# Optimization experiments

Measured on AMD Instinct MI355X. Metric: run time of the kernel, lower is better.

## Reference

```python
import jax, jax.numpy as jnp
import numpy as np

N = 50000      # nodes
E = 100000     # edges
F_NODE = 128
F_EDGE = 16
H = 64         # hidden_dim
OUT = 32
STEPS = 3
G = 64         # num_graphs (static; batch.max()+1 in torch)


def setup_inputs() -> dict:
    key = jax.random.key(0)
    ks = jax.random.split(key, 20)

    def lin(k, fin, fout):
        s = 1.0 / np.sqrt(fin)
        return jax.random.uniform(k, (fin, fout), jnp.float32, -s, s)

    def bias(k, fin, fout):
        s = 1.0 / np.sqrt(fin)
        return jax.random.uniform(k, (fout,), jnp.float32, -s, s)

    inp = {
        'x': jax.random.normal(ks[0], (N, F_NODE), jnp.float32),
        'edge_index': jax.random.randint(ks[1], (2, E), 0, N),
        'edge_attr': jax.random.normal(ks[2], (E, F_EDGE), jnp.float32),
        'batch': jnp.sort(jax.random.randint(ks[3], (N,), 0, G)),
        # node encoder
        'W_enc': lin(ks[4], F_NODE, H), 'b_enc': bias(ks[5], F_NODE, H),
        # edge_nn: Linear(F_EDGE,H) -> ReLU -> Linear(H, H*H)
        'W_e1': lin(ks[6], F_EDGE, H), 'b_e1': bias(ks[7], F_EDGE, H),
        'W_e2': lin(ks[8], H, H * H), 'b_e2': bias(ks[9], H, H * H),
        # GRUCell (torch layout: [3H, H])
        'W_ih': jax.random.uniform(ks[10], (3 * H, H), jnp.float32, -1/np.sqrt(H), 1/np.sqrt(H)),
        'W_hh': jax.random.uniform(ks[11], (3 * H, H), jnp.float32, -1/np.sqrt(H), 1/np.sqrt(H)),
        'b_ih': jax.random.uniform(ks[12], (3 * H,), jnp.float32, -1/np.sqrt(H), 1/np.sqrt(H)),
        'b_hh': jax.random.uniform(ks[13], (3 * H,), jnp.float32, -1/np.sqrt(H), 1/np.sqrt(H)),
        # readout MLP: Linear(H,H) -> ReLU -> Linear(H,OUT)
        'W_r1': lin(ks[14], H, H), 'b_r1': bias(ks[15], H, H),
        'W_r2': lin(ks[16], H, OUT), 'b_r2': bias(ks[17], H, OUT),
    }
    return inp


def gru_cell(m, h, W_ih, W_hh, b_ih, b_hh):
    gi = m @ W_ih.T + b_ih   # [N, 3H]
    gh = h @ W_hh.T + b_hh
    i_r, i_z, i_n = jnp.split(gi, 3, axis=-1)
    h_r, h_z, h_n = jnp.split(gh, 3, axis=-1)
    r = jax.nn.sigmoid(i_r + h_r)
    z = jax.nn.sigmoid(i_z + h_z)
    n = jnp.tanh(i_n + r * h_n)
    return (1.0 - z) * n + z * h


def reference(x, edge_index, edge_attr, batch, W_enc, b_enc, W_e1, b_e1,
              W_e2, b_e2, W_ih, W_hh, b_ih, b_hh, W_r1, b_r1, W_r2, b_r2):
    h = x @ W_enc + b_enc                                   # [N, H]
    src, dst = edge_index[0], edge_index[1]
    # edge-conditioned weight matrices (loop-invariant; compute once)
    ew = (jax.nn.relu(edge_attr @ W_e1 + b_e1) @ W_e2 + b_e2).reshape(E, H, H)
    for _ in range(STEPS):
        msg = jnp.einsum('eij,ej->ei', ew, h[src])          # per-edge matvec
        m_agg = jax.ops.segment_sum(msg, dst, num_segments=N)
        h = gru_cell(m_agg, h, W_ih, W_hh, b_ih, b_hh)
    g = jax.ops.segment_sum(h, batch, num_segments=G)       # sum readout
    return jax.nn.relu(g @ W_r1 + b_r1) @ W_r2 + b_r2
```

## Files before the change

### kernel.cpp

```cpp
#include <hip/hip_runtime.h>
#include <hip/hip_fp16.h>
#include <math.h>

#define NN 50000
#define NE 100000
#define FN 128
#define FE 16
#define HD 64
#define OUTD 32
#define NG 64
#define ZK 65
#define EB 256

typedef unsigned int uint;
typedef unsigned short ushort;
typedef __attribute__((ext_vector_type(8))) short short8;
typedef __attribute__((ext_vector_type(8))) _Float16 half8;
typedef __attribute__((ext_vector_type(2))) _Float16 half2v;
typedef __attribute__((ext_vector_type(16))) float f32x16;

static __device__ __forceinline__ ushort f2h(float f) {
    _Float16 h = (_Float16)f;
    return __builtin_bit_cast(ushort, h);
}
static __device__ __forceinline__ uint pkh2(float a, float b) {
    auto r = __builtin_amdgcn_cvt_pkrtz(a, b);
    return __builtin_bit_cast(uint, r);
}
static __device__ __forceinline__ uint hmul2u(uint a, uint b) {
    half2v x = __builtin_bit_cast(half2v, a);
    half2v y = __builtin_bit_cast(half2v, b);
    half2v r = x * y;
    return __builtin_bit_cast(uint, r);
}
static __device__ __forceinline__ half8 u4h8(uint4 u) {
    return __builtin_bit_cast(half8, u);
}
static __device__ __forceinline__ float fsigmoid(float x) {
    return 1.f / (1.f + __expf(-x));
}
static __device__ __forceinline__ float ftanh(float x) {
    float t = __expf(2.f * x);
    return 1.f - 2.f / (t + 1.f);
}

#define PREP_S0 (ZK * 4096)
#define PREP_S1 (256 * 128)
#define PREP_S2 (64 * 128)
__global__ void k_prep(const float* __restrict__ W_e2, const float* __restrict__ b_e2,
                       const float* __restrict__ W_ih, const float* __restrict__ W_hh,
                       const float* __restrict__ W_enc,
                       ushort* __restrict__ Wtb, ushort* __restrict__ Bg,
                       ushort* __restrict__ Wet) {
    int idx = blockIdx.x * 256 + threadIdx.x;
    if (idx < PREP_S0) {
        int k0 = idx >> 12, r = idx & 4095;
        int i = r >> 6, j = r & 63;
        float v = (k0 < 64) ? W_e2[k0 * 4096 + i * 64 + j] : b_e2[i * 64 + j];
        Wtb[idx] = f2h(v);
        return;
    }
    idx -= PREP_S0;
    if (idx < PREP_S1) {
        int n = idx >> 7, k = idx & 127;
        int g = n >> 6, i = n & 63;
        float v = 0.f;
        if (g == 0)      v = (k < 64) ? W_ih[i * 64 + k]         : W_hh[i * 64 + (k - 64)];
        else if (g == 1) v = (k < 64) ? W_ih[(64 + i) * 64 + k]  : W_hh[(64 + i) * 64 + (k - 64)];
        else if (g == 2) v = (k < 64) ? W_ih[(128 + i) * 64 + k] : 0.f;
        else             v = (k < 64) ? 0.f                      : W_hh[(128 + i) * 64 + (k - 64)];
        Bg[idx] = f2h(v);
        return;
    }
    idx -= PREP_S1;
    if (idx < PREP_S2) {
        int n = idx >> 7, k = idx & 127;
        Wet[idx] = f2h(W_enc[k * 64 + n]);
    }
}

#define NBENC ((NN + 127) / 128)
#define NBEDG ((NE + 255) / 256)
__global__ __launch_bounds__(256, 2)
void k_enc_edge(const float* __restrict__ x, const ushort* __restrict__ Wet,
                const float* __restrict__ b_enc,
                const float* __restrict__ ea, const float* __restrict__ W_e1,
                const float* __restrict__ b_e1,
                float* __restrict__ h, ushort* __restrict__ hb,
                ushort* __restrict__ zbT, float* __restrict__ magg) {
    int t = threadIdx.x;
    if (blockIdx.x < NBENC) {
        __shared__ __align__(16) ushort blds[64 * 128];
        int wave = t >> 6, lane = t & 63, l31 = lane & 31, lhi = lane >> 5;
        #pragma unroll
        for (int call = 0; call < 4; call++) {
            int slot = call * 256 + t;
            int n = slot >> 4, p = slot & 15;
            int ssrc = p ^ (n & 15);
            const ushort* src = Wet + n * 128 + ssrc * 8;
            __builtin_amdgcn_global_load_lds(
                (const __attribute__((address_space(1))) void*)src,
                (__attribute__((address_space(3))) void*)&blds[(size_t)slot * 8],
                16, 0, 0);
        }
        int node0 = blockIdx.x * 128 + wave * 32;
        int m = node0 + l31;
        int mc = (m < NN) ? m : NN - 1;
        uint4 afr[8];
        const float* xr = x + (size_t)mc * 128;
        #pragma unroll
        for (int ks = 0; ks < 8; ks++) {
            float4 v0 = *(const float4*)(xr + ks * 16 + lhi * 8);
            float4 v1 = *(const float4*)(xr + ks * 16 + lhi * 8 + 4);
            uint4 u;
            u.x = pkh2(v0.x, v0.y); u.y = pkh2(v0.z, v0.w);
            u.z = pkh2(v1.x, v1.y); u.w = pkh2(v1.z, v1.w);
            afr[ks] = u;
        }
        __syncthreads();
        #pragma unroll
        for (int ct = 0; ct < 2; ct++) {
            f32x16 acc = {0};
            int n = ct * 32 + l31;
            #pragma unroll
            for (int ks = 0; ks < 8; ks++) {
                int sp = (ks * 2 + lhi) ^ (n & 15);
                short8 bf = *(const short8*)&blds[n * 128 + sp * 8];
                acc = __builtin_amdgcn_mfma_f32_32x32x16_f16(
                    u4h8(afr[ks]), __builtin_bit_cast(half8, bf), acc, 0, 0, 0);
            }
            int o = ct * 32 + l31;
            float bias = b_enc[o];
            #pragma unroll
            for (int r = 0; r < 16; r++) {
                int row = (r & 3) + 8 * (r >> 2) + 4 * lhi;
                int node = node0 + row;
                if (node < NN) {
                    float v = acc[r] + bias;
                    h[node * 64 + o] = v;
                    hb[node * 64 + o] = f2h(v);
                    magg[node * 64 + o] = 0.f;
                }
            }
        }
    } else {
        __shared__ float Ws[16 * 64];
        __shared__ float b1s[64];
        for (int idx = t; idx < 1024; idx += 256) Ws[idx] = W_e1[idx];
        if (t < 64) b1s[t] = b_e1[t];
        __syncthreads();
        int e = (blockIdx.x - NBENC) * 256 + t;
        int ec = (e < NE) ? e : NE - 1;
        float eav[16];
        const float4* ep = (const float4*)(ea + ec * 16);
        #pragma unroll
        for (int q = 0; q < 4; q++) {
            float4 v = ep[q];
            eav[q * 4 + 0] = v.x; eav[q * 4 + 1] = v.y; eav[q * 4 + 2] = v.z; eav[q * 4 + 3] = v.w;
        }
        if (e >= NE) return;
        #pragma unroll 4
        for (int k = 0; k < 64; k++) {
            float acc = b1s[k];
            #pragma unroll
            for (int f = 0; f < 16; f++) acc += eav[f] * Ws[f * 64 + k];
            zbT[(size_t)k * NE + e] = f2h(fmaxf(acc, 0.f));
        }
    }
}

__global__ __launch_bounds__(256, 2)
void k_message(const ushort* __restrict__ zbT, const ushort* __restrict__ hb,
               const int* __restrict__ eidx, const ushort* __restrict__ Wtb,
               float* __restrict__ m_agg) {
    __shared__ __align__(16) ushort wlds[2][2 * 4096];
    __shared__ __align__(16) ushort zlds[64 * 256];
    __shared__ int sdst[256];

    int t = threadIdx.x;
    int wave = t >> 6, lane = t & 63;
    int l31 = lane & 31, lhi = lane >> 5;
    int eblk = blockIdx.x * EB;
    int e0 = eblk + wave * 64;

    {
        int e = eblk + t; if (e >= NE) e = NE - 1;
        sdst[t] = eidx[NE + e];
    }

    uint hw[2][16];
    #pragma unroll
    for (int mt = 0; mt < 2; mt++) {
        int e = e0 + mt * 32 + l31;
        int ec = (e < NE) ? e : NE - 1;
        int s = eidx[ec];
        const ushort* hrow = hb + (size_t)s * 64;
        #pragma unroll
        for (int c = 0; c < 4; c++) {
            uint4 v = *(const uint4*)(hrow + c * 16 + lhi * 8);
            hw[mt][c * 4 + 0] = v.x; hw[mt][c * 4 + 1] = v.y;
            hw[mt][c * 4 + 2] = v.z; hw[mt][c * 4 + 3] = v.w;
        }
    }

    #pragma unroll
    for (int call = 0; call < 8; call++) {
        int slot = call * 256 + t;
        int k0 = slot >> 5, p = slot & 31;
        const ushort* src = zbT + (size_t)k0 * NE + eblk + p * 8;
        __builtin_amdgcn_global_load_lds(
            (const __attribute__((address_space(1))) void*)src,
            (__attribute__((address_space(3))) void*)&zlds[(size_t)slot * 8],
            16, 0, 0);
    }

    auto stagew = [&](int slab0, int buf) {
        #pragma unroll
        for (int call = 0; call < 4; call++) {
            int slot = call * 256 + t;
            int slab = slab0 + (slot >> 9);
            if (slab > 64) slab = 64;
            int w = slot & 511;
            int i = w >> 3, jbp = w & 7;
            int jbg = jbp ^ (i & 7);
            const ushort* src = Wtb + (size_t)slab * 4096 + i * 64 + jbg * 8;
            __builtin_amdgcn_global_load_lds(
                (const __attribute__((address_space(1))) void*)src,
                (__attribute__((address_space(3))) void*)&wlds[buf][(size_t)(call * 256 + t) * 8],
                16, 0, 0);
        }
    };
    stagew(0, 0);

    f32x16 acc00 = {0}, acc01 = {0}, acc10 = {0}, acc11 = {0};

    for (int rnd = 0; rnd < 33; rnd++) {
        __syncthreads();
        int buf = rnd & 1;
        if (rnd < 32) stagew(2 * rnd + 2, buf ^ 1);
        int nk = (rnd < 32) ? 2 : 1;
        for (int kk = 0; kk < nk; kk++) {
            int k0 = 2 * rnd + kk;
            uint zz0, zz1;
            if (k0 < 64) {
                uint za = zlds[k0 * 256 + wave * 64 + l31];
                uint zb = zlds[k0 * 256 + wave * 64 + 32 + l31];
                zz0 = za | (za << 16);
                zz1 = zb | (zb << 16);
            } else {
                zz0 = 0x3C003C00u; zz1 = 0x3C003C00u;
            }
            const ushort* wb = &wlds[buf][kk * 4096];
            #pragma unroll
            for (int c = 0; c < 4; c++) {
                int jb = c * 2 + lhi;
                short8 b0r = *(const short8*)&wb[(l31 << 6) + ((jb ^ (l31 & 7)) << 3)];
                short8 b1r = *(const short8*)&wb[((32 + l31) << 6) + ((jb ^ (l31 & 7)) << 3)];
                uint4 au0, au1;
                au0.x = hmul2u(zz0, hw[0][c * 4 + 0]); au0.y = hmul2u(zz0, hw[0][c * 4 + 1]);
                au0.z = hmul2u(zz0, hw[0][c * 4 + 2]); au0.w = hmul2u(zz0, hw[0][c * 4 + 3]);
                au1.x = hmul2u(zz1, hw[1][c * 4 + 0]); au1.y = hmul2u(zz1, hw[1][c * 4 + 1]);
                au1.z = hmul2u(zz1, hw[1][c * 4 + 2]); au1.w = hmul2u(zz1, hw[1][c * 4 + 3]);
                half8 a0 = u4h8(au0), a1 = u4h8(au1);
                half8 b0 = __builtin_bit_cast(half8, b0r);
                half8 b1 = __builtin_bit_cast(half8, b1r);
                acc00 = __builtin_amdgcn_mfma_f32_32x32x16_f16(a0, b0, acc00, 0, 0, 0);
                acc01 = __builtin_amdgcn_mfma_f32_32x32x16_f16(a0, b1, acc01, 0, 0, 0);
                acc10 = __builtin_amdgcn_mfma_f32_32x32x16_f16(a1, b0, acc10, 0, 0, 0);
                acc11 = __builtin_amdgcn_mfma_f32_32x32x16_f16(a1, b1, acc11, 0, 0, 0);
            }
        }
    }

    #pragma unroll
    for (int r = 0; r < 16; r++) {
        int roff = (r & 3) + 8 * (r >> 2) + 4 * lhi;
        int eA = e0 + roff, eB = e0 + 32 + roff;
        if (eA < NE) {
            int d0 = sdst[wave * 64 + roff];
            atomicAdd(m_agg + (size_t)d0 * 64 + l31,      acc00[r]);
            atomicAdd(m_agg + (size_t)d0 * 64 + 32 + l31, acc01[r]);
        }
        if (eB < NE) {
            int d1 = sdst[wave * 64 + 32 + roff];
            atomicAdd(m_agg + (size_t)d1 * 64 + l31,      acc10[r]);
            atomicAdd(m_agg + (size_t)d1 * 64 + 32 + l31, acc11[r]);
        }
    }
}

__global__ __launch_bounds__(256, 2)
void k_gru(float* __restrict__ magg, const float* __restrict__ h,
           const ushort* __restrict__ hb, const ushort* __restrict__ Bg,
           const float* __restrict__ b_ih, const float* __restrict__ b_hh,
           float* __restrict__ h_out, ushort* __restrict__ hb_out, int zero_m) {
    __shared__ __align__(16) ushort blds[256 * 128];
    int t = threadIdx.x;
    int wave = t >> 6, lane = t & 63, l31 = lane & 31, lhi = lane >> 5;
    #pragma unroll
    for (int call = 0; call < 16; call++) {
        int slot = call * 256 + t;
        int n = slot >> 4, p = slot & 15;
        int ssrc = p ^ (n & 15);
        const ushort* src = Bg + n * 128 + ssrc * 8;
        __builtin_amdgcn_global_load_lds(
            (const __attribute__((address_space(1))) void*)src,
            (__attribute__((address_space(3))) void*)&blds[(size_t)slot * 8],
            16, 0, 0);
    }
    int node0 = blockIdx.x * 128 + wave * 32;
    int m = node0 + l31;
    int mc = (m < NN) ? m : NN - 1;
    uint4 afr[8];
    const float* mrow = magg + (size_t)mc * 64;
    #pragma unroll
    for (int ks = 0; ks < 4; ks++) {
        float4 v0 = *(const float4*)(mrow + ks * 16 + lhi * 8);
        float4 v1 = *(const float4*)(mrow + ks * 16 + lhi * 8 + 4);
        uint4 u;
        u.x = pkh2(v0.x, v0.y); u.y = pkh2(v0.z, v0.w);
        u.z = pkh2(v1.x, v1.y); u.w = pkh2(v1.z, v1.w);
        afr[ks] = u;
    }
    const ushort* hrow = hb + (size_t)mc * 64;
    #pragma unroll
    for (int ks = 4; ks < 8; ks++) {
        afr[ks] = *(const uint4*)(hrow + (ks - 4) * 16 + lhi * 8);
    }
    __syncthreads();
    if (zero_m) {
        float4 zz = {0.f, 0.f, 0.f, 0.f};
        float* mw = magg + (size_t)mc * 64;
        #pragma unroll
        for (int ks = 0; ks < 4; ks++) {
            *(float4*)(mw + ks * 16 + lhi * 8) = zz;
            *(float4*)(mw + ks * 16 + lhi * 8 + 4) = zz;
        }
    }
    #pragma unroll
    for (int ct = 0; ct < 2; ct++) {
        f32x16 aR = {0}, aZ = {0}, aI = {0}, aH = {0};
        int nR = 0   + ct * 32 + l31;
        int nZ = 64  + ct * 32 + l31;
        int nI = 128 + ct * 32 + l31;
        int nH = 192 + ct * 32 + l31;
        #pragma unroll
        for (int ks = 0; ks < 8; ks++) {
            int s = ks * 2 + lhi;
            half8 a = u4h8(afr[ks]);
            short8 bR = *(const short8*)&blds[nR * 128 + (s ^ (nR & 15)) * 8];
            short8 bZ = *(const short8*)&blds[nZ * 128 + (s ^ (nZ & 15)) * 8];
            short8 bI = *(const short8*)&blds[nI * 128 + (s ^ (nI & 15)) * 8];
            short8 bH = *(const short8*)&blds[nH * 128 + (s ^ (nH & 15)) * 8];
            aR = __builtin_amdgcn_mfma_f32_32x32x16_f16(a, __builtin_bit_cast(half8, bR), aR, 0, 0, 0);
            aZ = __builtin_amdgcn_mfma_f32_32x32x16_f16(a, __builtin_bit_cast(half8, bZ), aZ, 0, 0, 0);
            aI = __builtin_amdgcn_mfma_f32_32x32x16_f16(a, __builtin_bit_cast(half8, bI), aI, 0, 0, 0);
            aH = __builtin_amdgcn_mfma_f32_32x32x16_f16(a, __builtin_bit_cast(half8, bH), aH, 0, 0, 0);
        }
        int i = ct * 32 + l31;
        float brv = b_ih[i] + b_hh[i];
        float bzv = b_ih[64 + i] + b_hh[64 + i];
        float biv = b_ih[128 + i];
        float bhv = b_hh[128 + i];
        #pragma unroll
        for (int r = 0; r < 16; r++) {
            int row = (r & 3) + 8 * (r >> 2) + 4 * lhi;
            int node = node0 + row;
            if (node < NN) {
                float ho = h[node * 64 + i];
                float rg = fsigmoid(aR[r] + brv);
                float zg = fsigmoid(aZ[r] + bzv);
                float ng = ftanh(aI[r] + biv + rg * (aH[r] + bhv));
                float hv = (1.f - zg) * ng + zg * ho;
                h_out[node * 64 + i] = hv;
                hb_out[node * 64 + i] = f2h(hv);
            }
        }
    }
}

__global__ __launch_bounds__(256)
void k_scatter_g(const float* __restrict__ h, const int* __restrict__ batch,
                 float* __restrict__ g) {
    int t = threadIdx.x;
    int i = t & 63, sub = t >> 6;
    int n0 = blockIdx.x * 64 + sub * 16;
    if (n0 >= NN) return;
    float acc = 0.f;
    int curg = batch[n0];
    for (int q = 0; q < 16; q++) {
        int n = n0 + q;
        if (n >= NN) break;
        int gq = batch[n];
        if (gq != curg) {
            atomicAdd(&g[curg * 64 + i], acc);
            acc = 0.f; curg = gq;
        }
        acc += h[n * 64 + i];
    }
    atomicAdd(&g[curg * 64 + i], acc);
}

__global__ __launch_bounds__(1024)
void k_readout(const float* __restrict__ g, const float* __restrict__ W1, const float* __restrict__ b1,
               const float* __restrict__ W2, const float* __restrict__ b2, float* __restrict__ out) {
    __shared__ float gs[64 * 64];
    __shared__ float ts[64 * 64];
    int t = threadIdx.x;
    for (int idx = t; idx < 4096; idx += 1024) gs[idx] = g[idx];
    __syncthreads();
    for (int idx = t; idx < 4096; idx += 1024) {
        int r = idx >> 6, c = idx & 63;
        float acc = b1[c];
        #pragma unroll 8
        for (int k = 0; k < 64; k++) acc += gs[r * 64 + k] * W1[k * 64 + c];
        ts[idx] = fmaxf(acc, 0.f);
    }
    __syncthreads();
    for (int idx = t; idx < 2048; idx += 1024) {
        int r = idx >> 5, c = idx & 31;
        float acc = b2[c];
        #pragma unroll 8
        for (int k = 0; k < 64; k++) acc += ts[r * 64 + k] * W2[k * 32 + c];
        out[idx] = acc;
    }
}

extern "C" void kernel_launch(void* const* d_in, const int* in_sizes, int n_in,
                              void* d_out, int out_size, void* d_ws, size_t ws_size,
                              hipStream_t stream) {
    const float* x     = (const float*)d_in[0];
    const int*   ei    = (const int*)  d_in[1];
    const float* ea    = (const float*)d_in[2];
    const int*   batch = (const int*)  d_in[3];
    const float* W_enc = (const float*)d_in[4];
    const float* b_enc = (const float*)d_in[5];
    const float* W_e1  = (const float*)d_in[6];
    const float* b_e1  = (const float*)d_in[7];
    const float* W_e2  = (const float*)d_in[8];
    const float* b_e2  = (const float*)d_in[9];
    const float* W_ih  = (const float*)d_in[10];
    const float* W_hh  = (const float*)d_in[11];
    const float* b_ih  = (const float*)d_in[12];
    const float* b_hh  = (const float*)d_in[13];
    const float* W_r1  = (const float*)d_in[14];
    const float* b_r1  = (const float*)d_in[15];
    const float* W_r2  = (const float*)d_in[16];
    const float* b_r2  = (const float*)d_in[17];
    float* out = (float*)d_out;

    float* ws    = (float*)d_ws;
    float* h     = ws;
    float* h2    = h    + NN * 64;
    float* magg  = h2   + NN * 64;
    float* g     = magg + NN * 64;
    ushort* hb   = (ushort*)(g + NG * 64);
    ushort* hb2  = hb   + NN * 64;
    ushort* zbT  = hb2  + NN * 64;
    ushort* Wtb  = zbT  + (size_t)ZK * NE;
    ushort* Bgru = Wtb  + ZK * 4096;
    ushort* Wet  = Bgru + 256 * 128;

    hipLaunchKernelGGL(k_prep, dim3((PREP_S0 + PREP_S1 + PREP_S2 + 255) / 256), dim3(256), 0, stream,
                       W_e2, b_e2, W_ih, W_hh, W_enc, Wtb, Bgru, Wet);
    hipLaunchKernelGGL(k_enc_edge, dim3(NBENC + NBEDG), dim3(256), 0, stream,
                       x, Wet, b_enc, ea, W_e1, b_e1, h, hb, zbT, magg);

    float* hc = h;    float* hn = h2;
    ushort* hbc = hb; ushort* hbn = hb2;
    for (int s = 0; s < 3; s++) {
        hipLaunchKernelGGL(k_message, dim3((NE + EB - 1) / EB), dim3(256), 0, stream,
                           zbT, hbc, ei, Wtb, magg);
        hipLaunchKernelGGL(k_gru,     dim3((NN + 127) / 128), dim3(256), 0, stream,
                           magg, hc, hbc, Bgru, b_ih, b_hh, hn, hbn, (s < 2) ? 1 : 0);
        float* tf = hc; hc = hn; hn = tf;
        ushort* tb = hbc; hbc = hbn; hbn = tb;
    }

    hipMemsetAsync(g, 0, (size_t)NG * 64 * sizeof(float), stream);
    hipLaunchKernelGGL(k_scatter_g, dim3((NN + 63) / 64), dim3(256), 0, stream, hc, batch, g);
    hipLaunchKernelGGL(k_readout,   dim3(1), dim3(1024), 0, stream, g, W_r1, b_r1, W_r2, b_r2, out);
}
```

Measured before the change: 409.5 us.

## Split message k-reduction across two blocks, stream z slabs, drop fp32 h copies

The message kernel now launches twice as many blocks, each handling half of the 65 k-slabs for an edge block, with both halves accumulating into m_agg. The z-activation tile moves from a 32KB full-block LDS preload to per-round double-buffered staging, which cuts LDS use and lets the launch bound allow 4 blocks per CU. The fp32 hidden-state arrays are removed entirely; the GRU and readout read the fp16 copy, which saves memory traffic but carries the recurrent state in half precision. Splitting the reduction doubles the atomic scatter traffic into m_agg and repeats the source-row gathers in each half.

Result: slower. 468.1 us (+14.3%).

```diff
diff --git a/kernel.cpp b/kernel.cpp
--- a/kernel.cpp
+++ b/kernel.cpp
@@ -11,6 +11,7 @@
 #define NG 64
 #define ZK 65
 #define EB 256
+#define NBMSG ((NE + EB - 1) / EB)
 
 typedef unsigned int uint;
 typedef unsigned short ushort;
@@ -22,6 +23,9 @@
 static __device__ __forceinline__ ushort f2h(float f) {
     _Float16 h = (_Float16)f;
     return __builtin_bit_cast(ushort, h);
+}
+static __device__ __forceinline__ float h2f(ushort u) {
+    return (float)__builtin_bit_cast(_Float16, u);
 }
 static __device__ __forceinline__ uint pkh2(float a, float b) {
     auto r = __builtin_amdgcn_cvt_pkrtz(a, b);
@@ -86,7 +90,7 @@
                 const float* __restrict__ b_enc,
                 const float* __restrict__ ea, const float* __restrict__ W_e1,
                 const float* __restrict__ b_e1,
-                float* __restrict__ h, ushort* __restrict__ hb,
+                ushort* __restrict__ hb,
                 ushort* __restrict__ zbT, float* __restrict__ magg) {
     int t = threadIdx.x;
     if (blockIdx.x < NBENC) {
@@ -137,7 +141,6 @@
                 int node = node0 + row;
                 if (node < NN) {
                     float v = acc[r] + bias;
-                    h[node * 64 + o] = v;
                     hb[node * 64 + o] = f2h(v);
                     magg[node * 64 + o] = 0.f;
                 }
@@ -169,18 +172,25 @@
     }
 }
 
-__global__ __launch_bounds__(256, 2)
+__global__ __launch_bounds__(256, 4)
 void k_message(const ushort* __restrict__ zbT, const ushort* __restrict__ hb,
                const int* __restrict__ eidx, const ushort* __restrict__ Wtb,
                float* __restrict__ m_agg) {
     __shared__ __align__(16) ushort wlds[2][2 * 4096];
-    __shared__ __align__(16) ushort zlds[64 * 256];
+    __shared__ __align__(16) ushort zlds[2][2 * 256];
     __shared__ int sdst[256];
+
+    int bx = blockIdx.x;
+    int khalf = (bx >= NBMSG) ? 1 : 0;
+    int ebi = bx - khalf * NBMSG;
+    int kb = khalf ? 32 : 0;
+    int nslab = khalf ? 33 : 32;
+    int R = (nslab + 1) >> 1;
 
     int t = threadIdx.x;
     int wave = t >> 6, lane = t & 63;
     int l31 = lane & 31, lhi = lane >> 5;
-    int eblk = blockIdx.x * EB;
+    int eblk = ebi * EB;
     int e0 = eblk + wave * 64;
 
     {
@@ -203,22 +213,11 @@
         }
     }
 
-    #pragma unroll
-    for (int call = 0; call < 8; call++) {
-        int slot = call * 256 + t;
-        int k0 = slot >> 5, p = slot & 31;
-        const ushort* src = zbT + (size_t)k0 * NE + eblk + p * 8;
-        __builtin_amdgcn_global_load_lds(
-            (const __attribute__((address_space(1))) void*)src,
-            (__attribute__((address_space(3))) void*)&zlds[(size_t)slot * 8],
-            16, 0, 0);
-    }
-
-    auto stagew = [&](int slab0, int buf) {
+    auto stage = [&](int s0, int buf) {
         #pragma unroll
         for (int call = 0; call < 4; call++) {
             int slot = call * 256 + t;
-            int slab = slab0 + (slot >> 9);
+            int slab = s0 + (slot >> 9);
             if (slab > 64) slab = 64;
             int w = slot & 511;
             int i = w >> 3, jbp = w & 7;
@@ -226,25 +225,35 @@
             const ushort* src = Wtb + (size_t)slab * 4096 + i * 64 + jbg * 8;
             __builtin_amdgcn_global_load_lds(
                 (const __attribute__((address_space(1))) void*)src,
-                (__attribute__((address_space(3))) void*)&wlds[buf][(size_t)(call * 256 + t) * 8],
+                (__attribute__((address_space(3))) void*)&wlds[buf][(size_t)slot * 8],
                 16, 0, 0);
         }
+        if (t < 64) {
+            int k0 = s0 + (t >> 5);
+            if (k0 < 64) {
+                const ushort* src = zbT + (size_t)k0 * NE + eblk + (t & 31) * 8;
+                __builtin_amdgcn_global_load_lds(
+                    (const __attribute__((address_space(1))) void*)src,
+                    (__attribute__((address_space(3))) void*)&zlds[buf][(size_t)t * 8],
+                    16, 0, 0);
+            }
+        }
     };
-    stagew(0, 0);
+    stage(kb, 0);
 
     f32x16 acc00 = {0}, acc01 = {0}, acc10 = {0}, acc11 = {0};
 
-    for (int rnd = 0; rnd < 33; rnd++) {
+    for (int rnd = 0; rnd < R; rnd++) {
         __syncthreads();
         int buf = rnd & 1;
-        if (rnd < 32) stagew(2 * rnd + 2, buf ^ 1);
-        int nk = (rnd < 32) ? 2 : 1;
+        if (rnd + 1 < R) stage(kb + 2 * (rnd + 1), buf ^ 1);
+        int nk = nslab - 2 * rnd; if (nk > 2) nk = 2;
         for (int kk = 0; kk < nk; kk++) {
-            int k0 = 2 * rnd + kk;
+            int k0 = kb + 2 * rnd + kk;
             uint zz0, zz1;
             if (k0 < 64) {
-                uint za = zlds[k0 * 256 + wave * 64 + l31];
-                uint zb = zlds[k0 * 256 + wave * 64 + 32 + l31];
+                uint za = zlds[buf][kk * 256 + wave * 64 + l31];
+                uint zb = zlds[buf][kk * 256 + wave * 64 + 32 + l31];
                 zz0 = za | (za << 16);
                 zz1 = zb | (zb << 16);
             } else {
@@ -290,10 +299,10 @@
 }
 
 __global__ __launch_bounds__(256, 2)
-void k_gru(float* __restrict__ magg, const float* __restrict__ h,
+void k_gru(float* __restrict__ magg,
            const ushort* __restrict__ hb, const ushort* __restrict__ Bg,
            const float* __restrict__ b_ih, const float* __restrict__ b_hh,
-           float* __restrict__ h_out, ushort* __restrict__ hb_out, int zero_m) {
+           ushort* __restrict__ hb_out, int zero_m) {
     __shared__ __align__(16) ushort blds[256 * 128];
     int t = threadIdx.x;
     int wave = t >> 6, lane = t & 63, l31 = lane & 31, lhi = lane >> 5;
@@ -367,12 +376,11 @@
             int row = (r & 3) + 8 * (r >> 2) + 4 * lhi;
             int node = node0 + row;
             if (node < NN) {
-                float ho = h[node * 64 + i];
+                float ho = h2f(hb[node * 64 + i]);
                 float rg = fsigmoid(aR[r] + brv);
                 float zg = fsigmoid(aZ[r] + bzv);
                 float ng = ftanh(aI[r] + biv + rg * (aH[r] + bhv));
                 float hv = (1.f - zg) * ng + zg * ho;
-                h_out[node * 64 + i] = hv;
                 hb_out[node * 64 + i] = f2h(hv);
             }
         }
@@ -380,7 +388,7 @@
 }
 
 __global__ __launch_bounds__(256)
-void k_scatter_g(const float* __restrict__ h, const int* __restrict__ batch,
+void k_scatter_g(const ushort* __restrict__ hb, const int* __restrict__ batch,
                  float* __restrict__ g) {
     int t = threadIdx.x;
     int i = t & 63, sub = t >> 6;
@@ -396,7 +404,7 @@
             atomicAdd(&g[curg * 64 + i], acc);
             acc = 0.f; curg = gq;
         }
-        acc += h[n * 64 + i];
+        acc += h2f(hb[n * 64 + i]);
     }
     atomicAdd(&g[curg * 64 + i], acc);
 }
@@ -450,9 +458,7 @@
     float* out = (float*)d_out;
 
     float* ws    = (float*)d_ws;
-    float* h     = ws;
-    float* h2    = h    + NN * 64;
-    float* magg  = h2   + NN * 64;
+    float* magg  = ws;
     float* g     = magg + NN * 64;
     ushort* hb   = (ushort*)(g + NG * 64);
     ushort* hb2  = hb   + NN * 64;
@@ -464,20 +470,18 @@
     hipLaunchKernelGGL(k_prep, dim3((PREP_S0 + PREP_S1 + PREP_S2 + 255) / 256), dim3(256), 0, stream,
                        W_e2, b_e2, W_ih, W_hh, W_enc, Wtb, Bgru, Wet);
     hipLaunchKernelGGL(k_enc_edge, dim3(NBENC + NBEDG), dim3(256), 0, stream,
-                       x, Wet, b_enc, ea, W_e1, b_e1, h, hb, zbT, magg);
-
-    float* hc = h;    float* hn = h2;
+                       x, Wet, b_enc, ea, W_e1, b_e1, hb, zbT, magg);
+
     ushort* hbc = hb; ushort* hbn = hb2;
     for (int s = 0; s < 3; s++) {
-        hipLaunchKernelGGL(k_message, dim3((NE + EB - 1) / EB), dim3(256), 0, stream,
+        hipLaunchKernelGGL(k_message, dim3(2 * NBMSG), dim3(256), 0, stream,
                            zbT, hbc, ei, Wtb, magg);
         hipLaunchKernelGGL(k_gru,     dim3((NN + 127) / 128), dim3(256), 0, stream,
-                           magg, hc, hbc, Bgru, b_ih, b_hh, hn, hbn, (s < 2) ? 1 : 0);
-        float* tf = hc; hc = hn; hn = tf;
+                           magg, hbc, Bgru, b_ih, b_hh, hbn, (s < 2) ? 1 : 0);
         ushort* tb = hbc; hbc = hbn; hbn = tb;
     }
 
     hipMemsetAsync(g, 0, (size_t)NG * 64 * sizeof(float), stream);
-    hipLaunchKernelGGL(k_scatter_g, dim3((NN + 63) / 64), dim3(256), 0, stream, hc, batch, g);
+    hipLaunchKernelGGL(k_scatter_g, dim3((NN + 63) / 64), dim3(256), 0, stream, hbc, batch, g);
     hipLaunchKernelGGL(k_readout,   dim3(1), dim3(1024), 0, stream, g, W_r1, b_r1, W_r2, b_r2, out);
 }
```

## Drop fp32 hidden-state copy and pre-swizzle edge weight layout for LDS

Applied to the files above, without the earlier changes.

Removes the fp32 hidden-state buffers and keeps only the fp16 copy, which the GRU residual and the graph readout now read back as fp16. This cuts global writes and reads of a 50000x64 fp32 array per step. Separately, the edge-weight table is laid out in the prep kernel in a j-block-major order, so the message kernel can stage it with contiguous loads and read it without XOR swizzle arithmetic. The cost is lower precision for the carried hidden state, which accumulates fp16 rounding over the steps.

Measured after the change: 396.8 us. 1.03x faster.

```diff
diff --git a/kernel.cpp b/kernel.cpp
--- a/kernel.cpp
+++ b/kernel.cpp
@@ -11,6 +11,7 @@
 #define NG 64
 #define ZK 65
 #define EB 256
+#define NBMSG ((NE + EB - 1) / EB)
 
 typedef unsigned int uint;
 typedef unsigned short ushort;
@@ -22,6 +23,9 @@
 static __device__ __forceinline__ ushort f2h(float f) {
     _Float16 h = (_Float16)f;
     return __builtin_bit_cast(ushort, h);
+}
+static __device__ __forceinline__ float h2f(ushort u) {
+    return (float)__builtin_bit_cast(_Float16, u);
 }
 static __device__ __forceinline__ uint pkh2(float a, float b) {
     auto r = __builtin_amdgcn_cvt_pkrtz(a, b);
@@ -55,7 +59,9 @@
     int idx = blockIdx.x * 256 + threadIdx.x;
     if (idx < PREP_S0) {
         int k0 = idx >> 12, r = idx & 4095;
-        int i = r >> 6, j = r & 63;
+        int jb = r >> 9, rem = r & 511;
+        int i = rem >> 3, hh = rem & 7;
+        int j = jb * 8 + hh;
         float v = (k0 < 64) ? W_e2[k0 * 4096 + i * 64 + j] : b_e2[i * 64 + j];
         Wtb[idx] = f2h(v);
         return;
@@ -86,7 +92,7 @@
                 const float* __restrict__ b_enc,
                 const float* __restrict__ ea, const float* __restrict__ W_e1,
                 const float* __restrict__ b_e1,
-                float* __restrict__ h, ushort* __restrict__ hb,
+                ushort* __restrict__ hb,
                 ushort* __restrict__ zbT, float* __restrict__ magg) {
     int t = threadIdx.x;
     if (blockIdx.x < NBENC) {
@@ -137,7 +143,6 @@
                 int node = node0 + row;
                 if (node < NN) {
                     float v = acc[r] + bias;
-                    h[node * 64 + o] = v;
                     hb[node * 64 + o] = f2h(v);
                     magg[node * 64 + o] = 0.f;
                 }
@@ -220,13 +225,11 @@
             int slot = call * 256 + t;
             int slab = slab0 + (slot >> 9);
             if (slab > 64) slab = 64;
-            int w = slot & 511;
-            int i = w >> 3, jbp = w & 7;
-            int jbg = jbp ^ (i & 7);
-            const ushort* src = Wtb + (size_t)slab * 4096 + i * 64 + jbg * 8;
+            int wofs = slot & 511;
+            const ushort* src = Wtb + (size_t)slab * 4096 + wofs * 8;
             __builtin_amdgcn_global_load_lds(
                 (const __attribute__((address_space(1))) void*)src,
-                (__attribute__((address_space(3))) void*)&wlds[buf][(size_t)(call * 256 + t) * 8],
+                (__attribute__((address_space(3))) void*)&wlds[buf][(size_t)slot * 8],
                 16, 0, 0);
         }
     };
@@ -254,8 +257,8 @@
             #pragma unroll
             for (int c = 0; c < 4; c++) {
                 int jb = c * 2 + lhi;
-                short8 b0r = *(const short8*)&wb[(l31 << 6) + ((jb ^ (l31 & 7)) << 3)];
-                short8 b1r = *(const short8*)&wb[((32 + l31) << 6) + ((jb ^ (l31 & 7)) << 3)];
+                short8 b0r = *(const short8*)&wb[jb * 512 + l31 * 8];
+                short8 b1r = *(const short8*)&wb[jb * 512 + 256 + l31 * 8];
                 uint4 au0, au1;
                 au0.x = hmul2u(zz0, hw[0][c * 4 + 0]); au0.y = hmul2u(zz0, hw[0][c * 4 + 1]);
                 au0.z = hmul2u(zz0, hw[0][c * 4 + 2]); au0.w = hmul2u(zz0, hw[0][c * 4 + 3]);
@@ -290,10 +293,10 @@
 }
 
 __global__ __launch_bounds__(256, 2)
-void k_gru(float* __restrict__ magg, const float* __restrict__ h,
+void k_gru(float* __restrict__ magg,
            const ushort* __restrict__ hb, const ushort* __restrict__ Bg,
            const float* __restrict__ b_ih, const float* __restrict__ b_hh,
-           float* __restrict__ h_out, ushort* __restrict__ hb_out, int zero_m) {
+           ushort* __restrict__ hb_out, int zero_m) {
     __shared__ __align__(16) ushort blds[256 * 128];
     int t = threadIdx.x;
     int wave = t >> 6, lane = t & 63, l31 = lane & 31, lhi = lane >> 5;
@@ -367,12 +370,11 @@
             int row = (r & 3) + 8 * (r >> 2) + 4 * lhi;
             int node = node0 + row;
             if (node < NN) {
-                float ho = h[node * 64 + i];
+                float ho = h2f(hb[node * 64 + i]);
                 float rg = fsigmoid(aR[r] + brv);
                 float zg = fsigmoid(aZ[r] + bzv);
                 float ng = ftanh(aI[r] + biv + rg * (aH[r] + bhv));
                 float hv = (1.f - zg) * ng + zg * ho;
-                h_out[node * 64 + i] = hv;
                 hb_out[node * 64 + i] = f2h(hv);
             }
         }
@@ -380,7 +382,7 @@
 }
 
 __global__ __launch_bounds__(256)
-void k_scatter_g(const float* __restrict__ h, const int* __restrict__ batch,
+void k_scatter_g(const ushort* __restrict__ hb, const int* __restrict__ batch,
                  float* __restrict__ g) {
     int t = threadIdx.x;
     int i = t & 63, sub = t >> 6;
@@ -396,7 +398,7 @@
             atomicAdd(&g[curg * 64 + i], acc);
             acc = 0.f; curg = gq;
         }
-        acc += h[n * 64 + i];
+        acc += h2f(hb[n * 64 + i]);
     }
     atomicAdd(&g[curg * 64 + i], acc);
 }
@@ -450,9 +452,7 @@
     float* out = (float*)d_out;
 
     float* ws    = (float*)d_ws;
-    float* h     = ws;
-    float* h2    = h    + NN * 64;
-    float* magg  = h2   + NN * 64;
+    float* magg  = ws;
     float* g     = magg + NN * 64;
     ushort* hb   = (ushort*)(g + NG * 64);
     ushort* hb2  = hb   + NN * 64;
@@ -464,20 +464,18 @@
     hipLaunchKernelGGL(k_prep, dim3((PREP_S0 + PREP_S1 + PREP_S2 + 255) / 256), dim3(256), 0, stream,
                        W_e2, b_e2, W_ih, W_hh, W_enc, Wtb, Bgru, Wet);
     hipLaunchKernelGGL(k_enc_edge, dim3(NBENC + NBEDG), dim3(256), 0, stream,
-                       x, Wet, b_enc, ea, W_e1, b_e1, h, hb, zbT, magg);
-
-    float* hc = h;    float* hn = h2;
+                       x, Wet, b_enc, ea, W_e1, b_e1, hb, zbT, magg);
+
     ushort* hbc = hb; ushort* hbn = hb2;
     for (int s = 0; s < 3; s++) {
-        hipLaunchKernelGGL(k_message, dim3((NE + EB - 1) / EB), dim3(256), 0, stream,
+        hipLaunchKernelGGL(k_message, dim3(NBMSG), dim3(256), 0, stream,
                            zbT, hbc, ei, Wtb, magg);
         hipLaunchKernelGGL(k_gru,     dim3((NN + 127) / 128), dim3(256), 0, stream,
-                           magg, hc, hbc, Bgru, b_ih, b_hh, hn, hbn, (s < 2) ? 1 : 0);
-        float* tf = hc; hc = hn; hn = tf;
+                           magg, hbc, Bgru, b_ih, b_hh, hbn, (s < 2) ? 1 : 0);
         ushort* tb = hbc; hbc = hbn; hbn = tb;
     }
 
     hipMemsetAsync(g, 0, (size_t)NG * 64 * sizeof(float), stream);
-    hipLaunchKernelGGL(k_scatter_g, dim3((NN + 63) / 64), dim3(256), 0, stream, hc, batch, g);
+    hipLaunchKernelGGL(k_scatter_g, dim3((NN + 63) / 64), dim3(256), 0, stream, hbc, batch, g);
     hipLaunchKernelGGL(k_readout,   dim3(1), dim3(1024), 0, stream, g, W_r1, b_r1, W_r2, b_r2, out);
 }
```
